# Kernel optimization log

Hardware: AMD Instinct MI355X
Metric: run time of the kernel (lower is better)

Reference implementation:

```python
import jax, jax.numpy as jnp
import numpy as np

EMBED_DIM = 512
NUM_HEADS = 8
HEAD_DIM = EMBED_DIM // NUM_HEADS


def setup_inputs() -> dict:
    key = jax.random.key(0)
    ks = jax.random.split(key, 9)
    C = EMBED_DIM
    s = 1.0 / np.sqrt(C)
    x = jax.random.normal(ks[0], (1, 4096, C), dtype=jnp.float32)
    Wq = jax.random.uniform(ks[1], (C, C), jnp.float32, -s, s)
    bq = jax.random.uniform(ks[2], (C,), jnp.float32, -s, s)
    Wk = jax.random.uniform(ks[3], (C, C), jnp.float32, -s, s)
    bk = jax.random.uniform(ks[4], (C,), jnp.float32, -s, s)
    Wv = jax.random.uniform(ks[5], (C, C), jnp.float32, -s, s)
    bv = jax.random.uniform(ks[6], (C,), jnp.float32, -s, s)
    Wo = jax.random.uniform(ks[7], (C, C), jnp.float32, -s, s)
    bo = jax.random.uniform(ks[8], (C,), jnp.float32, -s, s)
    return {"x": x, "Wq": Wq, "bq": bq, "Wk": Wk, "bk": bk,
            "Wv": Wv, "bv": bv, "Wo": Wo, "bo": bo}


def reference(x, Wq, bq, Wk, bk, Wv, bv, Wo, bo):
    B, N, C = x.shape
    H, D = NUM_HEADS, HEAD_DIM
    # QKV projections, split into heads: [B, H, N, D]
    def proj(W, b):
        y = x @ W + b
        return y.reshape(B, N, H, D).transpose(0, 2, 1, 3)
    Q, K, V = proj(Wq, bq), proj(Wk, bk), proj(Wv, bv)
    # NOTE: original scales by 1/sqrt(embed_dim), NOT 1/sqrt(head_dim)
    scale = 1.0 / jnp.sqrt(jnp.float32(C)).astype(x.dtype)
    scores = jnp.einsum('bhnd,bhmd->bhnm', Q, K) * scale  # [B,H,N,N]
    attn = jax.nn.softmax(scores, axis=-1)
    out = jnp.einsum('bhnm,bhmd->bhnd', attn, V)  # [B,H,N,D]
    out = out.transpose(0, 2, 1, 3).reshape(B, N, C)
    return out @ Wo + bo
```

## Files before the change

### kernel.cpp

```cpp
#include <hip/hip_runtime.h>
#include <hip/hip_bf16.h>

#define SEQ 4096
#define CDIM 512
#define NHEAD 8
#define HDIM 64
#define KVB 64
#define NSPLIT 4
#define TILES_PER_SPLIT (SEQ / KVB / NSPLIT)

typedef __attribute__((ext_vector_type(8))) short bf16x8;
typedef __attribute__((ext_vector_type(4))) float f32x4;
typedef __attribute__((ext_vector_type(16))) float f32x16;

__device__ __forceinline__ short f2b(float f) {
  union { float f; unsigned u; } v; v.f = f;
  unsigned u = v.u;
  unsigned r = u + 0x7fffu + ((u >> 16) & 1u);
  return (short)(r >> 16);
}
__device__ __forceinline__ float b2f(short s) {
  union { unsigned u; float f; } v; v.u = ((unsigned)(unsigned short)s) << 16;
  return v.f;
}
__device__ __forceinline__ unsigned pk2(float a, float b) {
  union { __hip_bfloat162 h; unsigned u; } z;
  z.h = __float22bfloat162_rn(make_float2(a, b));
  return z.u;
}

__global__ __launch_bounds__(256) void prep_kernel(
    const float* __restrict__ x,
    const float* __restrict__ Wq, const float* __restrict__ Wk,
    const float* __restrict__ Wv, const float* __restrict__ Wo,
    short* __restrict__ xb,
    short* __restrict__ Wqt, short* __restrict__ Wkt,
    short* __restrict__ Wvt, short* __restrict__ Wot) {
  __shared__ short tile[32][33];
  int b = blockIdx.x, tid = threadIdx.x;
  if (b < 2048) {
    int i = (b * 256 + tid) * 4;
    float4 v = *(const float4*)(x + i);
    short4 o;
    o.x = f2b(v.x); o.y = f2b(v.y); o.z = f2b(v.z); o.w = f2b(v.w);
    *(short4*)(xb + i) = o;
    return;
  }
  int t = b - 2048;
  int mat = t >> 8; t &= 255;
  const float* W = mat == 0 ? Wq : mat == 1 ? Wk : mat == 2 ? Wv : Wo;
  short* Wt = mat == 0 ? Wqt : mat == 1 ? Wkt : mat == 2 ? Wvt : Wot;
  int n0 = (t & 15) * 32, k0 = (t >> 4) * 32;
  int tx = tid & 31, ty = tid >> 5;
  for (int i = 0; i < 32; i += 8)
    tile[ty + i][tx] = f2b(W[(size_t)(k0 + ty + i) * CDIM + n0 + tx]);
  __syncthreads();
  for (int i = 0; i < 32; i += 8)
    Wt[(size_t)(n0 + ty + i) * CDIM + k0 + tx] = tile[tx][ty + i];
}

#define GEMM128_CORE(Asrc, Btsrc)                                                          \
  f32x16 acc[2] = {};                                                                      \
  const int tid = threadIdx.x;                                                             \
  const int wid = tid >> 6, lane = tid & 63, l31 = lane & 31, hi = lane >> 5;              \
  const int wr = wid >> 1, wc = wid & 1;                                                   \
  for (int kt = 0; kt < CDIM; kt += 64) {                                                  \
    __syncthreads();                                                                       \
    _Pragma("unroll")                                                                      \
    for (int i = 0; i < 4; ++i) {                                                          \
      int idx = i * 256 + tid, row = idx >> 3, seg = idx & 7;                              \
      int sc = (seg ^ (row & 7)) * 8;                                                      \
      __builtin_amdgcn_global_load_lds(                                                    \
          (const __attribute__((address_space(1))) void*)(Asrc + (size_t)(m0 + row) * CDIM + kt + sc), \
          (__attribute__((address_space(3))) void*)(As + idx * 8), 16, 0, 0);              \
    }                                                                                      \
    _Pragma("unroll")                                                                      \
    for (int i = 0; i < 2; ++i) {                                                          \
      int idx = i * 256 + tid, row = idx >> 3, seg = idx & 7;                              \
      int sc = (seg ^ (row & 7)) * 8;                                                      \
      __builtin_amdgcn_global_load_lds(                                                    \
          (const __attribute__((address_space(1))) void*)(Btsrc + (size_t)(n0 + row) * CDIM + kt + sc), \
          (__attribute__((address_space(3))) void*)(Bs + idx * 8), 16, 0, 0);              \
    }                                                                                      \
    __syncthreads();                                                                       \
    _Pragma("unroll")                                                                      \
    for (int ks = 0; ks < 4; ++ks) {                                                       \
      int brow = wc * 32 + l31;                                                            \
      bf16x8 bfr = *(const bf16x8*)(Bs + brow * 64 + ((ks * 16 + hi * 8) ^ ((brow & 7) * 8))); \
      _Pragma("unroll")                                                                    \
      for (int ai = 0; ai < 2; ++ai) {                                                     \
        int arow = wr * 64 + ai * 32 + l31;                                                \
        bf16x8 afr = *(const bf16x8*)(As + arow * 64 + ((ks * 16 + hi * 8) ^ ((arow & 7) * 8))); \
        acc[ai] = __builtin_amdgcn_mfma_f32_32x32x16_bf16(afr, bfr, acc[ai], 0, 0, 0);     \
      }                                                                                    \
    }                                                                                      \
  }

__global__ __launch_bounds__(256) void qkv128_kernel(
    const short* __restrict__ A,
    const short* __restrict__ Wqt, const short* __restrict__ Wkt, const short* __restrict__ Wvt,
    const float* __restrict__ bq, const float* __restrict__ bk, const float* __restrict__ bv,
    short* __restrict__ Qb, short* __restrict__ Kb, short* __restrict__ Vtb) {
  __shared__ __align__(16) short As[128 * 64];
  __shared__ __align__(16) short Bs[64 * 64];
  const int z = blockIdx.z;
  const short* Bt = z == 0 ? Wqt : z == 1 ? Wkt : Wvt;
  const float* bias = z == 0 ? bq : z == 1 ? bk : bv;
  const int m0 = blockIdx.x * 128, n0 = blockIdx.y * 64;
  GEMM128_CORE(A, Bt)
  const int ncol = n0 + wc * 32 + l31;
  const float bn = bias[ncol];
  if (z != 2) {
    short* D = z == 0 ? Qb : Kb;
#pragma unroll
    for (int ai = 0; ai < 2; ++ai)
#pragma unroll
      for (int r = 0; r < 16; ++r) {
        int m = m0 + wr * 64 + ai * 32 + (r & 3) + 8 * (r >> 2) + 4 * hi;
        D[(size_t)m * CDIM + ncol] = f2b(acc[ai][r] + bn);
      }
  } else {
#pragma unroll
    for (int ai = 0; ai < 2; ++ai)
#pragma unroll
      for (int r = 0; r < 16; ++r) {
        int m = m0 + wr * 64 + ai * 32 + (r & 3) + 8 * (r >> 2) + 4 * hi;
        Vtb[(size_t)ncol * SEQ + m] = f2b(acc[ai][r] + bn);
      }
  }
}

__global__ __launch_bounds__(256) void out128_kernel(
    const short* __restrict__ A, const short* __restrict__ Bt,
    const float* __restrict__ bias, float* __restrict__ out) {
  __shared__ __align__(16) short As[128 * 64];
  __shared__ __align__(16) short Bs[64 * 64];
  const int m0 = blockIdx.x * 128, n0 = blockIdx.y * 64;
  GEMM128_CORE(A, Bt)
  const int ncol = n0 + wc * 32 + l31;
  const float bn = bias[ncol];
#pragma unroll
  for (int ai = 0; ai < 2; ++ai)
#pragma unroll
    for (int r = 0; r < 16; ++r) {
      int m = m0 + wr * 64 + ai * 32 + (r & 3) + 8 * (r >> 2) + 4 * hi;
      out[(size_t)m * CDIM + ncol] = acc[ai][r] + bn;
    }
}

__global__ __launch_bounds__(512, 4) void attn_kernel(
    const short* __restrict__ Qb,
    const short* __restrict__ Kb,
    const short* __restrict__ Vtb,
    short* __restrict__ Op0, short* __restrict__ Op1,
    short* __restrict__ Op2, short* __restrict__ Op3,
    float* __restrict__ lpart) {
  __shared__ __align__(16) char arena[49152];
  __shared__ float lzp[4][32];
  short* KsB = (short*)arena;
  short* VsB = (short*)(arena + 24576);
  const int bid = blockIdx.x;
  const int h = bid & 7;
  const int rest = bid >> 3;
  const int split = rest & 3;
  const int q0 = (rest >> 2) * 128;
  const int kvbase = split * (TILES_PER_SPLIT * KVB);
  const int tid = threadIdx.x;
  const int wid = tid >> 6, lane = tid & 63;
  const int l31 = lane & 31, hi = lane >> 5;
  const int rh = wid >> 1, kq = wid & 1;
  const float scale2 = 0.06375872274f;

  short* Opart = split == 0 ? Op0 : split == 1 ? Op1 : split == 2 ? Op2 : Op3;

  bf16x8 qf[4];
  {
    int qrow = q0 + rh * 32 + l31;
#pragma unroll
    for (int kst = 0; kst < 4; ++kst) {
      bf16x8 q = *(const bf16x8*)(Qb + (size_t)qrow * CDIM + h * 64 + kst * 16 + hi * 8);
#pragma unroll
      for (int i = 0; i < 8; ++i) q[i] = f2b(b2f(q[i]) * scale2);
      qf[kst] = q;
    }
  }

  const int srow = tid >> 3;
  const int scol8 = 8 * ((tid & 7) ^ (srow & 7));
  const short* kstage = Kb + (size_t)(kvbase + srow) * CDIM + h * 64 + scol8;
  const short* vstage = Vtb + (size_t)(h * 64 + srow) * SEQ + kvbase + scol8;
  auto stage = [&](short* sK, short* sV) {
    __builtin_amdgcn_global_load_lds(
        (const __attribute__((address_space(1))) void*)kstage,
        (__attribute__((address_space(3))) void*)(sK + tid * 8), 16, 0, 0);
    __builtin_amdgcn_global_load_lds(
        (const __attribute__((address_space(1))) void*)vstage,
        (__attribute__((address_space(3))) void*)(sV + tid * 8), 16, 0, 0);
    kstage += KVB * CDIM;
    vstage += KVB;
  };

  f32x16 osum[2] = {};
  float lsum = 0.f;
  unsigned w[8];

  auto softmax = [&](f32x16& s) {
    float ls0 = 0.f, ls1 = 0.f;
#pragma unroll
    for (int m = 0; m < 8; ++m) {
      float p0 = __builtin_amdgcn_exp2f(s[2 * m]);
      float p1 = __builtin_amdgcn_exp2f(s[2 * m + 1]);
      ls0 += p0; ls1 += p1;
      w[m] = pk2(p0, p1);
    }
    lsum += ls0 + ls1;
  };

  auto phase = [&](const short* vbuf, const short* kbuf, short* sK, short* sV, bool do_st) {
    if (do_st) stage(sK, sV);
    union { unsigned u[4]; bf16x8 v; } pf0, pf1;
#if __has_builtin(__builtin_amdgcn_permlane32_swap)
    {
      auto a0 = __builtin_amdgcn_permlane32_swap(w[0], w[2], false, false);
      auto a1 = __builtin_amdgcn_permlane32_swap(w[1], w[3], false, false);
      auto a2 = __builtin_amdgcn_permlane32_swap(w[4], w[6], false, false);
      auto a3 = __builtin_amdgcn_permlane32_swap(w[5], w[7], false, false);
      pf0.u[0] = a0[0]; pf0.u[1] = a1[0]; pf0.u[2] = a0[1]; pf0.u[3] = a1[1];
      pf1.u[0] = a2[0]; pf1.u[1] = a3[0]; pf1.u[2] = a2[1]; pf1.u[3] = a3[1];
    }
#else
    {
      unsigned t0 = hi ? w[0] : w[2], t1 = hi ? w[1] : w[3];
      unsigned t2 = hi ? w[4] : w[6], t3 = hi ? w[5] : w[7];
      unsigned r0 = __shfl_xor(t0, 32), r1 = __shfl_xor(t1, 32);
      unsigned r2 = __shfl_xor(t2, 32), r3 = __shfl_xor(t3, 32);
      pf0.u[0] = hi ? r0 : w[0]; pf0.u[1] = hi ? r1 : w[1];
      pf0.u[2] = hi ? w[2] : r0; pf0.u[3] = hi ? w[3] : r1;
      pf1.u[0] = hi ? r2 : w[4]; pf1.u[1] = hi ? r3 : w[5];
      pf1.u[2] = hi ? w[6] : r2; pf1.u[3] = hi ? w[7] : r3;
    }
#endif
    f32x16 s = {};
    __builtin_amdgcn_s_setprio(1);
#pragma unroll
    for (int kst = 0; kst < 4; ++kst) {
      int row = kq * 32 + l31;
      bf16x8 kf = *(const bf16x8*)(kbuf + row * 64 + ((kst * 16 + hi * 8) ^ ((row & 7) * 8)));
      s = __builtin_amdgcn_mfma_f32_32x32x16_bf16(kf, qf[kst], s, 0, 0, 0);
    }
#pragma unroll
    for (int dm = 0; dm < 2; ++dm) {
      int vrow = dm * 32 + l31;
      bf16x8 vf0 = *(const bf16x8*)(vbuf + vrow * 64 + ((kq * 32 + hi * 8) ^ ((vrow & 7) * 8)));
      osum[dm] = __builtin_amdgcn_mfma_f32_32x32x16_bf16(vf0, pf0.v, osum[dm], 0, 0, 0);
      bf16x8 vf1 = *(const bf16x8*)(vbuf + vrow * 64 + ((kq * 32 + 16 + hi * 8) ^ ((vrow & 7) * 8)));
      osum[dm] = __builtin_amdgcn_mfma_f32_32x32x16_bf16(vf1, pf1.v, osum[dm], 0, 0, 0);
    }
    __builtin_amdgcn_s_setprio(0);
    softmax(s);
    __syncthreads();
  };

  stage(KsB, VsB);
  __syncthreads();
  stage(KsB + 4096, VsB + 4096);
  {
    f32x16 s = {};
#pragma unroll
    for (int kst = 0; kst < 4; ++kst) {
      int row = kq * 32 + l31;
      bf16x8 kf = *(const bf16x8*)(KsB + row * 64 + ((kst * 16 + hi * 8) ^ ((row & 7) * 8)));
      s = __builtin_amdgcn_mfma_f32_32x32x16_bf16(kf, qf[kst], s, 0, 0, 0);
    }
    softmax(s);
  }
  __syncthreads();

  for (int t = 0; t < TILES_PER_SPLIT - 1; t += 3) {
    phase(VsB,        KsB + 4096, KsB + 8192, VsB + 8192, t + 2 < TILES_PER_SPLIT);
    phase(VsB + 4096, KsB + 8192, KsB,        VsB,        t + 3 < TILES_PER_SPLIT);
    phase(VsB + 8192, KsB,        KsB + 4096, VsB + 4096, t + 4 < TILES_PER_SPLIT);
  }

  {
    union { unsigned u[4]; bf16x8 v; } pf0, pf1;
#if __has_builtin(__builtin_amdgcn_permlane32_swap)
    auto a0 = __builtin_amdgcn_permlane32_swap(w[0], w[2], false, false);
    auto a1 = __builtin_amdgcn_permlane32_swap(w[1], w[3], false, false);
    auto a2 = __builtin_amdgcn_permlane32_swap(w[4], w[6], false, false);
    auto a3 = __builtin_amdgcn_permlane32_swap(w[5], w[7], false, false);
    pf0.u[0] = a0[0]; pf0.u[1] = a1[0]; pf0.u[2] = a0[1]; pf0.u[3] = a1[1];
    pf1.u[0] = a2[0]; pf1.u[1] = a3[0]; pf1.u[2] = a2[1]; pf1.u[3] = a3[1];
#else
    unsigned t0 = hi ? w[0] : w[2], t1 = hi ? w[1] : w[3];
    unsigned t2 = hi ? w[4] : w[6], t3 = hi ? w[5] : w[7];
    unsigned r0 = __shfl_xor(t0, 32), r1 = __shfl_xor(t1, 32);
    unsigned r2 = __shfl_xor(t2, 32), r3 = __shfl_xor(t3, 32);
    pf0.u[0] = hi ? r0 : w[0]; pf0.u[1] = hi ? r1 : w[1];
    pf0.u[2] = hi ? w[2] : r0; pf0.u[3] = hi ? w[3] : r1;
    pf1.u[0] = hi ? r2 : w[4]; pf1.u[1] = hi ? r3 : w[5];
    pf1.u[2] = hi ? w[6] : r2; pf1.u[3] = hi ? w[7] : r3;
#endif
#pragma unroll
    for (int dm = 0; dm < 2; ++dm) {
      int vrow = dm * 32 + l31;
      bf16x8 vf0 = *(const bf16x8*)(VsB + vrow * 64 + ((kq * 32 + hi * 8) ^ ((vrow & 7) * 8)));
      osum[dm] = __builtin_amdgcn_mfma_f32_32x32x16_bf16(vf0, pf0.v, osum[dm], 0, 0, 0);
      bf16x8 vf1 = *(const bf16x8*)(VsB + vrow * 64 + ((kq * 32 + 16 + hi * 8) ^ ((vrow & 7) * 8)));
      osum[dm] = __builtin_amdgcn_mfma_f32_32x32x16_bf16(vf1, pf1.v, osum[dm], 0, 0, 0);
    }
  }

  lsum += __shfl_xor(lsum, 32);

  __syncthreads();
  float* bufA = (float*)arena;
#define OD(dm, r) ((dm) * 32 + ((r) & 3) + 8 * ((r) >> 2) + 4 * hi)
#define OADDR(dm, r) (rh * 2112 + OD(dm, r) * 33 + l31)
  if (kq == 1) {
    if (hi == 0) lzp[rh][l31] = lsum;
#pragma unroll
    for (int dm = 0; dm < 2; ++dm)
#pragma unroll
      for (int r = 0; r < 16; ++r) bufA[OADDR(dm, r)] = osum[dm][r];
  }
  __syncthreads();
  if (kq == 0) {
#pragma unroll
    for (int dm = 0; dm < 2; ++dm)
#pragma unroll
      for (int r = 0; r < 16; ++r) {
        float v = osum[dm][r] + bufA[OADDR(dm, r)];
        bufA[OADDR(dm, r)] = v;
      }
    float lt = lsum + lzp[rh][l31];
    if (hi == 0)
      lpart[(size_t)(split * NHEAD + h) * SEQ + q0 + rh * 32 + l31] = lt;
  }
  __syncthreads();
#undef OD
#undef OADDR

  {
    int q_ = tid >> 2;
    int dc = (tid & 3) * 16;
    int qr = q_ >> 5, ql = q_ & 31;
    short ov[16];
#pragma unroll
    for (int i = 0; i < 16; ++i)
      ov[i] = f2b(bufA[qr * 2112 + (dc + i) * 33 + ql]);
    *(bf16x8*)(Opart + (size_t)(q0 + q_) * CDIM + h * 64 + dc) = *(bf16x8*)(ov);
    *(bf16x8*)(Opart + (size_t)(q0 + q_) * CDIM + h * 64 + dc + 8) = *(bf16x8*)(ov + 8);
  }
}

__global__ __launch_bounds__(256) void combine_kernel(
    const short* __restrict__ p0, const short* __restrict__ p1,
    const short* __restrict__ p2, const short* __restrict__ p3,
    const float* __restrict__ lpart, short* __restrict__ Ab) {
  int t = blockIdx.x * 256 + threadIdx.x;
  size_t base = (size_t)t * 8;
  int q = (int)(base >> 9), c = (int)(base & 511), h = c >> 6;
  float l = lpart[(size_t)(0 * NHEAD + h) * SEQ + q] +
            lpart[(size_t)(1 * NHEAD + h) * SEQ + q] +
            lpart[(size_t)(2 * NHEAD + h) * SEQ + q] +
            lpart[(size_t)(3 * NHEAD + h) * SEQ + q];
  float rinv = 1.f / l;
  bf16x8 a0 = *(const bf16x8*)(p0 + base);
  bf16x8 a1 = *(const bf16x8*)(p1 + base);
  bf16x8 a2 = *(const bf16x8*)(p2 + base);
  bf16x8 a3 = *(const bf16x8*)(p3 + base);
  short ov[8];
#pragma unroll
  for (int i = 0; i < 8; ++i)
    ov[i] = f2b((b2f(a0[i]) + b2f(a1[i]) + b2f(a2[i]) + b2f(a3[i])) * rinv);
  *(bf16x8*)(Ab + base) = *(bf16x8*)(ov);
}

extern "C" void kernel_launch(void* const* d_in, const int* in_sizes, int n_in,
                              void* d_out, int out_size, void* d_ws, size_t ws_size,
                              hipStream_t stream) {
  const float* x  = (const float*)d_in[0];
  const float* Wq = (const float*)d_in[1];
  const float* bq = (const float*)d_in[2];
  const float* Wk = (const float*)d_in[3];
  const float* bk = (const float*)d_in[4];
  const float* Wv = (const float*)d_in[5];
  const float* bv = (const float*)d_in[6];
  const float* Wo = (const float*)d_in[7];
  const float* bo = (const float*)d_in[8];
  float* out = (float*)d_out;

  short* ws = (short*)d_ws;
  size_t off = 0;
  short* xb  = ws + off; off += (size_t)SEQ * CDIM;
  short* Wqt = ws + off; off += (size_t)CDIM * CDIM;
  short* Wkt = ws + off; off += (size_t)CDIM * CDIM;
  short* Wvt = ws + off; off += (size_t)CDIM * CDIM;
  short* Wot = ws + off; off += (size_t)CDIM * CDIM;
  short* Qb  = ws + off; off += (size_t)SEQ * CDIM;
  short* Kb  = ws + off; off += (size_t)SEQ * CDIM;
  short* Vtb = ws + off; off += (size_t)CDIM * SEQ;
  short* Ab  = ws + off; off += (size_t)SEQ * CDIM;
  short* Op1 = ws + off; off += (size_t)SEQ * CDIM;
  short* Op2 = ws + off; off += (size_t)SEQ * CDIM;
  short* Op3 = ws + off; off += (size_t)SEQ * CDIM;
  float* lpart = (float*)(ws + off); off += (size_t)NSPLIT * NHEAD * SEQ * 2;
  short* Op0 = xb;

  prep_kernel<<<2048 + 4 * 256, 256, 0, stream>>>(x, Wq, Wk, Wv, Wo, xb, Wqt, Wkt, Wvt, Wot);
  qkv128_kernel<<<dim3(SEQ / 128, CDIM / 64, 3), 256, 0, stream>>>(
      xb, Wqt, Wkt, Wvt, bq, bk, bv, Qb, Kb, Vtb);
  attn_kernel<<<(SEQ / 128) * NHEAD * NSPLIT, 512, 0, stream>>>(
      Qb, Kb, Vtb, Op0, Op1, Op2, Op3, lpart);
  combine_kernel<<<SEQ * CDIM / 8 / 256, 256, 0, stream>>>(Op0, Op1, Op2, Op3, lpart, Ab);
  out128_kernel<<<dim3(SEQ / 128, CDIM / 64), 256, 0, stream>>>(Ab, Wot, bo, out);
}
```

Measured before the change: 81.77 us.

## Halve KV splits and fuse split-combine into output projection GEMM

Reduces the attention KV split count from 4 to 2, which halves the partial-output buffers and the traffic spent writing and rereading them. The separate combine kernel is removed. Its work (summing the partials, normalising by the summed row sums, converting to bf16) now happens inside the output projection's A-tile load, replacing the async global-to-LDS copy there with register loads and LDS stores. The attention tile loop is restructured for the new tile count (32 tiles), with a tail phase and a final buffer index. The cost is half as many attention blocks, which lowers parallelism, and the out GEMM recomputes the normalisation once per N-block, eight times in total.

```diff
diff --git a/kernel.cpp b/kernel.cpp
--- a/kernel.cpp
+++ b/kernel.cpp
@@ -6,7 +6,7 @@
 #define NHEAD 8
 #define HDIM 64
 #define KVB 64
-#define NSPLIT 4
+#define NSPLIT 2
 #define TILES_PER_SPLIT (SEQ / KVB / NSPLIT)
 
 typedef __attribute__((ext_vector_type(8))) short bf16x8;
@@ -59,43 +59,6 @@
     Wt[(size_t)(n0 + ty + i) * CDIM + k0 + tx] = tile[tx][ty + i];
 }
 
-#define GEMM128_CORE(Asrc, Btsrc)                                                          \
-  f32x16 acc[2] = {};                                                                      \
-  const int tid = threadIdx.x;                                                             \
-  const int wid = tid >> 6, lane = tid & 63, l31 = lane & 31, hi = lane >> 5;              \
-  const int wr = wid >> 1, wc = wid & 1;                                                   \
-  for (int kt = 0; kt < CDIM; kt += 64) {                                                  \
-    __syncthreads();                                                                       \
-    _Pragma("unroll")                                                                      \
-    for (int i = 0; i < 4; ++i) {                                                          \
-      int idx = i * 256 + tid, row = idx >> 3, seg = idx & 7;                              \
-      int sc = (seg ^ (row & 7)) * 8;                                                      \
-      __builtin_amdgcn_global_load_lds(                                                    \
-          (const __attribute__((address_space(1))) void*)(Asrc + (size_t)(m0 + row) * CDIM + kt + sc), \
-          (__attribute__((address_space(3))) void*)(As + idx * 8), 16, 0, 0);              \
-    }                                                                                      \
-    _Pragma("unroll")                                                                      \
-    for (int i = 0; i < 2; ++i) {                                                          \
-      int idx = i * 256 + tid, row = idx >> 3, seg = idx & 7;                              \
-      int sc = (seg ^ (row & 7)) * 8;                                                      \
-      __builtin_amdgcn_global_load_lds(                                                    \
-          (const __attribute__((address_space(1))) void*)(Btsrc + (size_t)(n0 + row) * CDIM + kt + sc), \
-          (__attribute__((address_space(3))) void*)(Bs + idx * 8), 16, 0, 0);              \
-    }                                                                                      \
-    __syncthreads();                                                                       \
-    _Pragma("unroll")                                                                      \
-    for (int ks = 0; ks < 4; ++ks) {                                                       \
-      int brow = wc * 32 + l31;                                                            \
-      bf16x8 bfr = *(const bf16x8*)(Bs + brow * 64 + ((ks * 16 + hi * 8) ^ ((brow & 7) * 8))); \
-      _Pragma("unroll")                                                                    \
-      for (int ai = 0; ai < 2; ++ai) {                                                     \
-        int arow = wr * 64 + ai * 32 + l31;                                                \
-        bf16x8 afr = *(const bf16x8*)(As + arow * 64 + ((ks * 16 + hi * 8) ^ ((arow & 7) * 8))); \
-        acc[ai] = __builtin_amdgcn_mfma_f32_32x32x16_bf16(afr, bfr, acc[ai], 0, 0, 0);     \
-      }                                                                                    \
-    }                                                                                      \
-  }
-
 __global__ __launch_bounds__(256) void qkv128_kernel(
     const short* __restrict__ A,
     const short* __restrict__ Wqt, const short* __restrict__ Wkt, const short* __restrict__ Wvt,
@@ -107,7 +70,41 @@
   const short* Bt = z == 0 ? Wqt : z == 1 ? Wkt : Wvt;
   const float* bias = z == 0 ? bq : z == 1 ? bk : bv;
   const int m0 = blockIdx.x * 128, n0 = blockIdx.y * 64;
-  GEMM128_CORE(A, Bt)
+  f32x16 acc[2] = {};
+  const int tid = threadIdx.x;
+  const int wid = tid >> 6, lane = tid & 63, l31 = lane & 31, hi = lane >> 5;
+  const int wr = wid >> 1, wc = wid & 1;
+  for (int kt = 0; kt < CDIM; kt += 64) {
+    __syncthreads();
+#pragma unroll
+    for (int i = 0; i < 4; ++i) {
+      int idx = i * 256 + tid, row = idx >> 3, seg = idx & 7;
+      int sc = (seg ^ (row & 7)) * 8;
+      __builtin_amdgcn_global_load_lds(
+          (const __attribute__((address_space(1))) void*)(A + (size_t)(m0 + row) * CDIM + kt + sc),
+          (__attribute__((address_space(3))) void*)(As + idx * 8), 16, 0, 0);
+    }
+#pragma unroll
+    for (int i = 0; i < 2; ++i) {
+      int idx = i * 256 + tid, row = idx >> 3, seg = idx & 7;
+      int sc = (seg ^ (row & 7)) * 8;
+      __builtin_amdgcn_global_load_lds(
+          (const __attribute__((address_space(1))) void*)(Bt + (size_t)(n0 + row) * CDIM + kt + sc),
+          (__attribute__((address_space(3))) void*)(Bs + idx * 8), 16, 0, 0);
+    }
+    __syncthreads();
+#pragma unroll
+    for (int ks = 0; ks < 4; ++ks) {
+      int brow = wc * 32 + l31;
+      bf16x8 bfr = *(const bf16x8*)(Bs + brow * 64 + ((ks * 16 + hi * 8) ^ ((brow & 7) * 8)));
+#pragma unroll
+      for (int ai = 0; ai < 2; ++ai) {
+        int arow = wr * 64 + ai * 32 + l31;
+        bf16x8 afr = *(const bf16x8*)(As + arow * 64 + ((ks * 16 + hi * 8) ^ ((arow & 7) * 8)));
+        acc[ai] = __builtin_amdgcn_mfma_f32_32x32x16_bf16(afr, bfr, acc[ai], 0, 0, 0);
+      }
+    }
+  }
   const int ncol = n0 + wc * 32 + l31;
   const float bn = bias[ncol];
   if (z != 2) {
@@ -131,12 +128,52 @@
 }
 
 __global__ __launch_bounds__(256) void out128_kernel(
-    const short* __restrict__ A, const short* __restrict__ Bt,
-    const float* __restrict__ bias, float* __restrict__ out) {
+    const short* __restrict__ p0, const short* __restrict__ p1,
+    const float* __restrict__ lpart,
+    const short* __restrict__ Bt, const float* __restrict__ bias,
+    float* __restrict__ out) {
   __shared__ __align__(16) short As[128 * 64];
   __shared__ __align__(16) short Bs[64 * 64];
   const int m0 = blockIdx.x * 128, n0 = blockIdx.y * 64;
-  GEMM128_CORE(A, Bt)
+  f32x16 acc[2] = {};
+  const int tid = threadIdx.x;
+  const int wid = tid >> 6, lane = tid & 63, l31 = lane & 31, hi = lane >> 5;
+  const int wr = wid >> 1, wc = wid & 1;
+  for (int kt = 0; kt < CDIM; kt += 64) {
+    __syncthreads();
+#pragma unroll
+    for (int i = 0; i < 4; ++i) {
+      int idx = i * 256 + tid, row = idx >> 3, seg = idx & 7;
+      int q = m0 + row, col = kt + seg * 8, h = col >> 6;
+      float rinv = 1.f / (lpart[(size_t)h * SEQ + q] + lpart[(size_t)(NHEAD + h) * SEQ + q]);
+      bf16x8 a0 = *(const bf16x8*)(p0 + (size_t)q * CDIM + col);
+      bf16x8 a1 = *(const bf16x8*)(p1 + (size_t)q * CDIM + col);
+      short ov[8];
+#pragma unroll
+      for (int e = 0; e < 8; ++e) ov[e] = f2b((b2f(a0[e]) + b2f(a1[e])) * rinv);
+      *(bf16x8*)(As + row * 64 + ((seg * 8) ^ ((row & 7) * 8))) = *(bf16x8*)ov;
+    }
+#pragma unroll
+    for (int i = 0; i < 2; ++i) {
+      int idx = i * 256 + tid, row = idx >> 3, seg = idx & 7;
+      int sc = (seg ^ (row & 7)) * 8;
+      __builtin_amdgcn_global_load_lds(
+          (const __attribute__((address_space(1))) void*)(Bt + (size_t)(n0 + row) * CDIM + kt + sc),
+          (__attribute__((address_space(3))) void*)(Bs + idx * 8), 16, 0, 0);
+    }
+    __syncthreads();
+#pragma unroll
+    for (int ks = 0; ks < 4; ++ks) {
+      int brow = wc * 32 + l31;
+      bf16x8 bfr = *(const bf16x8*)(Bs + brow * 64 + ((ks * 16 + hi * 8) ^ ((brow & 7) * 8)));
+#pragma unroll
+      for (int ai = 0; ai < 2; ++ai) {
+        int arow = wr * 64 + ai * 32 + l31;
+        bf16x8 afr = *(const bf16x8*)(As + arow * 64 + ((ks * 16 + hi * 8) ^ ((arow & 7) * 8)));
+        acc[ai] = __builtin_amdgcn_mfma_f32_32x32x16_bf16(afr, bfr, acc[ai], 0, 0, 0);
+      }
+    }
+  }
   const int ncol = n0 + wc * 32 + l31;
   const float bn = bias[ncol];
 #pragma unroll
@@ -153,7 +190,6 @@
     const short* __restrict__ Kb,
     const short* __restrict__ Vtb,
     short* __restrict__ Op0, short* __restrict__ Op1,
-    short* __restrict__ Op2, short* __restrict__ Op3,
     float* __restrict__ lpart) {
   __shared__ __align__(16) char arena[49152];
   __shared__ float lzp[4][32];
@@ -162,8 +198,8 @@
   const int bid = blockIdx.x;
   const int h = bid & 7;
   const int rest = bid >> 3;
-  const int split = rest & 3;
-  const int q0 = (rest >> 2) * 128;
+  const int split = rest & 1;
+  const int q0 = (rest >> 1) * 128;
   const int kvbase = split * (TILES_PER_SPLIT * KVB);
   const int tid = threadIdx.x;
   const int wid = tid >> 6, lane = tid & 63;
@@ -171,7 +207,7 @@
   const int rh = wid >> 1, kq = wid & 1;
   const float scale2 = 0.06375872274f;
 
-  short* Opart = split == 0 ? Op0 : split == 1 ? Op1 : split == 2 ? Op2 : Op3;
+  short* Opart = split == 0 ? Op0 : Op1;
 
   bf16x8 qf[4];
   {
@@ -216,30 +252,30 @@
     lsum += ls0 + ls1;
   };
 
+  auto mk_pf = [&](unsigned* u0, unsigned* u1) {
+#if __has_builtin(__builtin_amdgcn_permlane32_swap)
+    auto a0 = __builtin_amdgcn_permlane32_swap(w[0], w[2], false, false);
+    auto a1 = __builtin_amdgcn_permlane32_swap(w[1], w[3], false, false);
+    auto a2 = __builtin_amdgcn_permlane32_swap(w[4], w[6], false, false);
+    auto a3 = __builtin_amdgcn_permlane32_swap(w[5], w[7], false, false);
+    u0[0] = a0[0]; u0[1] = a1[0]; u0[2] = a0[1]; u0[3] = a1[1];
+    u1[0] = a2[0]; u1[1] = a3[0]; u1[2] = a2[1]; u1[3] = a3[1];
+#else
+    unsigned t0 = hi ? w[0] : w[2], t1 = hi ? w[1] : w[3];
+    unsigned t2 = hi ? w[4] : w[6], t3 = hi ? w[5] : w[7];
+    unsigned r0 = __shfl_xor(t0, 32), r1 = __shfl_xor(t1, 32);
+    unsigned r2 = __shfl_xor(t2, 32), r3 = __shfl_xor(t3, 32);
+    u0[0] = hi ? r0 : w[0]; u0[1] = hi ? r1 : w[1];
+    u0[2] = hi ? w[2] : r0; u0[3] = hi ? w[3] : r1;
+    u1[0] = hi ? r2 : w[4]; u1[1] = hi ? r3 : w[5];
+    u1[2] = hi ? w[6] : r2; u1[3] = hi ? w[7] : r3;
+#endif
+  };
+
   auto phase = [&](const short* vbuf, const short* kbuf, short* sK, short* sV, bool do_st) {
     if (do_st) stage(sK, sV);
     union { unsigned u[4]; bf16x8 v; } pf0, pf1;
-#if __has_builtin(__builtin_amdgcn_permlane32_swap)
-    {
-      auto a0 = __builtin_amdgcn_permlane32_swap(w[0], w[2], false, false);
-      auto a1 = __builtin_amdgcn_permlane32_swap(w[1], w[3], false, false);
-      auto a2 = __builtin_amdgcn_permlane32_swap(w[4], w[6], false, false);
-      auto a3 = __builtin_amdgcn_permlane32_swap(w[5], w[7], false, false);
-      pf0.u[0] = a0[0]; pf0.u[1] = a1[0]; pf0.u[2] = a0[1]; pf0.u[3] = a1[1];
-      pf1.u[0] = a2[0]; pf1.u[1] = a3[0]; pf1.u[2] = a2[1]; pf1.u[3] = a3[1];
-    }
-#else
-    {
-      unsigned t0 = hi ? w[0] : w[2], t1 = hi ? w[1] : w[3];
-      unsigned t2 = hi ? w[4] : w[6], t3 = hi ? w[5] : w[7];
-      unsigned r0 = __shfl_xor(t0, 32), r1 = __shfl_xor(t1, 32);
-      unsigned r2 = __shfl_xor(t2, 32), r3 = __shfl_xor(t3, 32);
-      pf0.u[0] = hi ? r0 : w[0]; pf0.u[1] = hi ? r1 : w[1];
-      pf0.u[2] = hi ? w[2] : r0; pf0.u[3] = hi ? w[3] : r1;
-      pf1.u[0] = hi ? r2 : w[4]; pf1.u[1] = hi ? r3 : w[5];
-      pf1.u[2] = hi ? w[6] : r2; pf1.u[3] = hi ? w[7] : r3;
-    }
-#endif
+    mk_pf(pf0.u, pf1.u);
     f32x16 s = {};
     __builtin_amdgcn_s_setprio(1);
 #pragma unroll
@@ -276,37 +312,23 @@
   }
   __syncthreads();
 
-  for (int t = 0; t < TILES_PER_SPLIT - 1; t += 3) {
-    phase(VsB,        KsB + 4096, KsB + 8192, VsB + 8192, t + 2 < TILES_PER_SPLIT);
-    phase(VsB + 4096, KsB + 8192, KsB,        VsB,        t + 3 < TILES_PER_SPLIT);
-    phase(VsB + 8192, KsB,        KsB + 4096, VsB + 4096, t + 4 < TILES_PER_SPLIT);
-  }
+  for (int t = 0; t + 3 < TILES_PER_SPLIT; t += 3) {
+    phase(VsB,        KsB + 4096, KsB + 8192, VsB + 8192, true);
+    phase(VsB + 4096, KsB + 8192, KsB,        VsB,        true);
+    phase(VsB + 8192, KsB,        KsB + 4096, VsB + 4096, true);
+  }
+  phase(VsB, KsB + 4096, KsB, VsB, false);
 
   {
     union { unsigned u[4]; bf16x8 v; } pf0, pf1;
-#if __has_builtin(__builtin_amdgcn_permlane32_swap)
-    auto a0 = __builtin_amdgcn_permlane32_swap(w[0], w[2], false, false);
-    auto a1 = __builtin_amdgcn_permlane32_swap(w[1], w[3], false, false);
-    auto a2 = __builtin_amdgcn_permlane32_swap(w[4], w[6], false, false);
-    auto a3 = __builtin_amdgcn_permlane32_swap(w[5], w[7], false, false);
-    pf0.u[0] = a0[0]; pf0.u[1] = a1[0]; pf0.u[2] = a0[1]; pf0.u[3] = a1[1];
-    pf1.u[0] = a2[0]; pf1.u[1] = a3[0]; pf1.u[2] = a2[1]; pf1.u[3] = a3[1];
-#else
-    unsigned t0 = hi ? w[0] : w[2], t1 = hi ? w[1] : w[3];
-    unsigned t2 = hi ? w[4] : w[6], t3 = hi ? w[5] : w[7];
-    unsigned r0 = __shfl_xor(t0, 32), r1 = __shfl_xor(t1, 32);
-    unsigned r2 = __shfl_xor(t2, 32), r3 = __shfl_xor(t3, 32);
-    pf0.u[0] = hi ? r0 : w[0]; pf0.u[1] = hi ? r1 : w[1];
-    pf0.u[2] = hi ? w[2] : r0; pf0.u[3] = hi ? w[3] : r1;
-    pf1.u[0] = hi ? r2 : w[4]; pf1.u[1] = hi ? r3 : w[5];
-    pf1.u[2] = hi ? w[6] : r2; pf1.u[3] = hi ? w[7] : r3;
-#endif
+    mk_pf(pf0.u, pf1.u);
+    const short* vb = VsB + 4096;
 #pragma unroll
     for (int dm = 0; dm < 2; ++dm) {
       int vrow = dm * 32 + l31;
-      bf16x8 vf0 = *(const bf16x8*)(VsB + vrow * 64 + ((kq * 32 + hi * 8) ^ ((vrow & 7) * 8)));
+      bf16x8 vf0 = *(const bf16x8*)(vb + vrow * 64 + ((kq * 32 + hi * 8) ^ ((vrow & 7) * 8)));
       osum[dm] = __builtin_amdgcn_mfma_f32_32x32x16_bf16(vf0, pf0.v, osum[dm], 0, 0, 0);
-      bf16x8 vf1 = *(const bf16x8*)(VsB + vrow * 64 + ((kq * 32 + 16 + hi * 8) ^ ((vrow & 7) * 8)));
+      bf16x8 vf1 = *(const bf16x8*)(vb + vrow * 64 + ((kq * 32 + 16 + hi * 8) ^ ((vrow & 7) * 8)));
       osum[dm] = __builtin_amdgcn_mfma_f32_32x32x16_bf16(vf1, pf1.v, osum[dm], 0, 0, 0);
     }
   }
@@ -352,29 +374,6 @@
     *(bf16x8*)(Opart + (size_t)(q0 + q_) * CDIM + h * 64 + dc) = *(bf16x8*)(ov);
     *(bf16x8*)(Opart + (size_t)(q0 + q_) * CDIM + h * 64 + dc + 8) = *(bf16x8*)(ov + 8);
   }
-}
-
-__global__ __launch_bounds__(256) void combine_kernel(
-    const short* __restrict__ p0, const short* __restrict__ p1,
-    const short* __restrict__ p2, const short* __restrict__ p3,
-    const float* __restrict__ lpart, short* __restrict__ Ab) {
-  int t = blockIdx.x * 256 + threadIdx.x;
-  size_t base = (size_t)t * 8;
-  int q = (int)(base >> 9), c = (int)(base & 511), h = c >> 6;
-  float l = lpart[(size_t)(0 * NHEAD + h) * SEQ + q] +
-            lpart[(size_t)(1 * NHEAD + h) * SEQ + q] +
-            lpart[(size_t)(2 * NHEAD + h) * SEQ + q] +
-            lpart[(size_t)(3 * NHEAD + h) * SEQ + q];
-  float rinv = 1.f / l;
-  bf16x8 a0 = *(const bf16x8*)(p0 + base);
-  bf16x8 a1 = *(const bf16x8*)(p1 + base);
-  bf16x8 a2 = *(const bf16x8*)(p2 + base);
-  bf16x8 a3 = *(const bf16x8*)(p3 + base);
-  short ov[8];
-#pragma unroll
-  for (int i = 0; i < 8; ++i)
-    ov[i] = f2b((b2f(a0[i]) + b2f(a1[i]) + b2f(a2[i]) + b2f(a3[i])) * rinv);
-  *(bf16x8*)(Ab + base) = *(bf16x8*)(ov);
 }
 
 extern "C" void kernel_launch(void* const* d_in, const int* in_sizes, int n_in,
@@ -401,10 +400,7 @@
   short* Qb  = ws + off; off += (size_t)SEQ * CDIM;
   short* Kb  = ws + off; off += (size_t)SEQ * CDIM;
   short* Vtb = ws + off; off += (size_t)CDIM * SEQ;
-  short* Ab  = ws + off; off += (size_t)SEQ * CDIM;
   short* Op1 = ws + off; off += (size_t)SEQ * CDIM;
-  short* Op2 = ws + off; off += (size_t)SEQ * CDIM;
-  short* Op3 = ws + off; off += (size_t)SEQ * CDIM;
   float* lpart = (float*)(ws + off); off += (size_t)NSPLIT * NHEAD * SEQ * 2;
   short* Op0 = xb;
 
@@ -412,7 +408,7 @@
   qkv128_kernel<<<dim3(SEQ / 128, CDIM / 64, 3), 256, 0, stream>>>(
       xb, Wqt, Wkt, Wvt, bq, bk, bv, Qb, Kb, Vtb);
   attn_kernel<<<(SEQ / 128) * NHEAD * NSPLIT, 512, 0, stream>>>(
-      Qb, Kb, Vtb, Op0, Op1, Op2, Op3, lpart);
-  combine_kernel<<<SEQ * CDIM / 8 / 256, 256, 0, stream>>>(Op0, Op1, Op2, Op3, lpart, Ab);
-  out128_kernel<<<dim3(SEQ / 128, CDIM / 64), 256, 0, stream>>>(Ab, Wot, bo, out);
-}
+      Qb, Kb, Vtb, Op0, Op1, lpart);
+  out128_kernel<<<dim3(SEQ / 128, CDIM / 64), 256, 0, stream>>>(
+      Op0, Op1, lpart, Wot, bo, out);
+}
```

Result: slower. 101.4 us (+24.1%).
